# Performance work log

Measured on AMD Instinct MI355X. Metric: run time of the kernel, lower is better.

Reference implementation:

```python
import jax, jax.numpy as jnp
import numpy as np

N = 256
L = 1024
ALPHA = 0.5  # GBT_alpha: bilinear transform


def _hippo_legs(n):
    # HiPPO-LegS: A[i,k] = -sqrt(2i+1)sqrt(2k+1) if i>k; -(i+1) if i==k; 0 else
    q = np.arange(n, dtype=np.float64)
    r = np.sqrt(2.0 * q + 1.0)
    A = r[:, None] * r[None, :] * (q[:, None] > q[None, :])
    A = -(A + np.diag(q + 1.0))
    B = r[:, None]  # (N, 1)
    return A.astype(np.float32), B.astype(np.float32)


def setup_inputs() -> dict:
    key = jax.random.key(0)
    k_f, = jax.random.split(key, 1)
    A_np, B_np = _hippo_legs(N)
    return {
        "f": jax.random.normal(k_f, (L, 1), dtype=jnp.float32),
        "init_state": jnp.zeros((N, 1), dtype=jnp.float32),
        "A": jnp.asarray(A_np),
        "B": jnp.asarray(B_np),
    }


def reference(f, init_state, A, B):
    n = A.shape[0]
    seq_len = f.shape[0]
    C = jnp.ones((n,), dtype=jnp.float32)  # module's self.C
    I = jnp.eye(n, dtype=jnp.float32)

    # Per-step discretization: at step i (1-indexed), step_size = 1/i.
    step_sizes = 1.0 / jnp.arange(1, seq_len + 1, dtype=jnp.float32)  # (L,)

    def discretize(ss):
        # part1 = I - ss*alpha*A ; part2 = I + ss*(1-alpha)*A
        P1 = I - ss * ALPHA * A
        P2 = I + ss * (1.0 - ALPHA) * A
        # lstsq on an invertible square system == solve
        Ad = jnp.linalg.solve(P1, P2)          # (N, N)
        Bd = ss * jnp.linalg.solve(P1, B)      # (N, 1)
        return Ad, Bd

    GBT_A, GBT_B = jax.vmap(discretize)(step_sizes)  # (L,N,N), (L,N,1)

    f_scalar = f[:, 0]  # loop uses f[i-1][0]

    def step(c_prev, inp):
        Ad, Bd, fk = inp
        c = Ad @ c_prev + Bd * fk  # (N, 1)
        y = C @ c                  # (1,)
        return c, (c, y)

    _, (c_all, y_all) = jax.lax.scan(step, init_state, (GBT_A, GBT_B, f_scalar))
    # c_all: (L, N, 1) stacked hidden states; y_all: (L, 1)
    return c_all, y_all, GBT_A, GBT_B
```

## Files before the change

### kernel.cpp

```cpp
#include <hip/hip_runtime.h>

#define LSEQ 1024
#define NDIM 256

#define O_C 0
#define O_Y (LSEQ * NDIM)
#define O_A (O_Y + LSEQ)
#define O_B (O_A + (size_t)LSEQ * NDIM * NDIM)

#define RING 128
#define NGRP 136

typedef float v4f __attribute__((ext_vector_type(4)));

static __device__ __forceinline__ float frcp(float x) {
    return __builtin_amdgcn_rcpf(x);
}

static __device__ __forceinline__ float dpp_shr1(float inject, float src) {
    int r = __builtin_amdgcn_update_dpp(
        __float_as_int(inject), __float_as_int(src),
        0x138 , 0xF, 0xF, false);
    return __int_as_float(r);
}

__global__ __launch_bounds__(256) void hippo_main(
    const float* __restrict__ f,
    const float* __restrict__ init_state,
    const float* __restrict__ Bvec,
    float* __restrict__ out)
{
    const int tid = threadIdx.x;
    const int bid = blockIdx.x;

    if (bid == 0) {
        __shared__ float c_ring[RING * NDIM];
        __shared__ float y_lds[LSEQ];
        __shared__ float f_lds[LSEQ];

        for (int i = tid; i < LSEQ; i += 256) f_lds[i] = f[i];
        __syncthreads();

        if (tid < 64) {
            const int l = tid;
            float rr[4], cc[4];
            #pragma unroll
            for (int e = 0; e < 4; ++e) {
                rr[e] = Bvec[4 * l + e];
                cc[e] = init_state[4 * l + e];
            }
            const float base1 = (float)(4 * l + 1);

            float T = 0.0f, S = 0.0f, ssf = 0.0f, yacc = 0.0f;
            float fcur = f_lds[l];
            float fnxt = f_lds[64 + l];

            for (int grp = 0; grp <= NGRP; ++grp) {
                if (grp < NGRP) {
                    const int tb = grp * 8;
                    if ((tb & 63) == 0 && tb) {
                        fcur = fnxt;
                        int nb = tb + 64;
                        fnxt = f_lds[(nb < LSEQ ? nb : 0) + l];
                    }
                    const int fb = tb & 63;

                    #pragma unroll
                    for (int g = 0; g < 8; ++g) {
                        const int t = tb + g;
                        float ft = __int_as_float(
                            __builtin_amdgcn_readlane(__float_as_int(fcur), fb + g));

                        const int k0 = t - l;
                        const float h  = 0.5f * frcp((float)(k0 + 1));
                        const float h0 = 0.5f * frcp((float)(t + 1));
                        const float ssf0 = 2.0f * h0 * ft;

                        T    = dpp_shr1(0.0f, T);
                        S    = dpp_shr1(0.0f, S);
                        yacc = dpp_shr1(0.0f, yacc);
                        ssf  = dpp_shr1(ssf0, ssf);

                        if (k0 >= 0 && k0 < LSEQ) {
                            #pragma unroll
                            for (int e = 0; e < 4; ++e) {
                                float d    = fmaf(h, base1 + (float)e, 1.0f);
                                float invd = frcp(d);
                                float w = fmaf(2.0f - d, cc[e],
                                               rr[e] * fmaf(-h, T, ssf));
                                T = fmaf(rr[e], cc[e], T);
                                float num = fmaf(-h * rr[e], S, w);
                                float cn  = num * invd;
                                S = fmaf(rr[e], cn, S);
                                cc[e] = cn;
                            }
                            yacc += (cc[0] + cc[1]) + (cc[2] + cc[3]);
                            const int slot = t & (RING - 1);
                            v4f cv = { cc[0], cc[1], cc[2], cc[3] };
                            *reinterpret_cast<v4f*>(
                                &c_ring[slot * NDIM + 4 * l]) = cv;
                            if (l == 63) y_lds[k0] = yacc;
                        }
                    }
                }
                __syncthreads();
            }
        } else {
            const int wave = tid >> 6;
            const int lane = tid & 63;
            for (int grp = 0; grp <= NGRP; ++grp) {
                const int tb = grp * 8;
                #pragma unroll
                for (int ri = 0; ri < 8; ++ri) {
                    if (ri / 3 != wave - 1) continue;
                    int r = tb - 71 + ri;
                    if (r < 0 || r >= LSEQ) continue;
                    int slot = (r + lane) & (RING - 1);
                    v4f d = *reinterpret_cast<const v4f*>(
                        &c_ring[slot * NDIM + 4 * lane]);
                    *reinterpret_cast<v4f*>(
                        out + O_C + (size_t)r * NDIM + 4 * lane) = d;
                    if (lane == 0) out[O_Y + r] = y_lds[r];
                }
                __syncthreads();
            }
        }
    } else {
        const int k = bid - 1;
        const int lane = tid & 63;
        const int wave = tid >> 6;
        const float kp = (float)(k + 1);
        const float ss = 1.0f / kp;
        const float h  = 0.5f * ss;

        __shared__ float s_r[NDIM], s_invd[NDIM], s_rowco[NDIM], s_g[NDIM], s_diag[NDIM];
        {
            int i = tid;
            float r    = Bvec[i];
            float d    = fmaf(h, (float)(i + 1), 1.0f);
            float invd = 1.0f / d;
            s_r[i]     = r;
            s_invd[i]  = invd;
            s_rowco[i] = -2.0f * h * r * invd;
            s_g[i]     = (1.0f - h * (float)i) * invd;
            s_diag[i]  = fmaf(2.0f, invd, -1.0f);
        }
        __syncthreads();

        {
            float Pi = 1.0f;
            for (int j = 0; j < NDIM - 1; ++j) {
                float gj = s_g[j];
                Pi *= (j < tid) ? gj : 1.0f;
            }
            float* outB = out + O_B + (size_t)k * NDIM;
            outB[tid] = ss * s_r[tid] * s_invd[tid] * Pi;
        }

        float colc[4], Scol[4] = {0.f, 0.f, 0.f, 0.f};
        #pragma unroll
        for (int e = 0; e < 4; ++e) {
            int j = 4 * lane + e;
            colc[e] = s_r[j] * s_invd[j];
        }

        const int i0 = wave * 64;
        for (int i = 0; i < i0; ++i) {
            float g = s_g[i];
            #pragma unroll
            for (int e = 0; e < 4; ++e) {
                int j = 4 * lane + e;
                if (j < i)       Scol[e] *= g;
                else if (j == i) Scol[e] = colc[e];
            }
        }
        float* outA = out + O_A + (size_t)k * (NDIM * NDIM) + 4 * lane;
        for (int i = i0; i < i0 + 64; ++i) {
            float rowco = s_rowco[i];
            float g     = s_g[i];
            float dg    = s_diag[i];
            float v[4];
            #pragma unroll
            for (int e = 0; e < 4; ++e) {
                int j = 4 * lane + e;
                if (j < i) {
                    v[e] = rowco * Scol[e];
                    Scol[e] *= g;
                } else if (j == i) {
                    v[e] = dg;
                    Scol[e] = colc[e];
                } else {
                    v[e] = 0.0f;
                }
            }
            v4f vv = { v[0], v[1], v[2], v[3] };
            __builtin_nontemporal_store(
                vv, reinterpret_cast<v4f*>(outA + (size_t)i * NDIM));
        }
    }
}

extern "C" void kernel_launch(void* const* d_in, const int* in_sizes, int n_in,
                              void* d_out, int out_size, void* d_ws, size_t ws_size,
                              hipStream_t stream) {
    (void)in_sizes; (void)n_in; (void)d_ws; (void)ws_size; (void)out_size;
    const float* f    = (const float*)d_in[0];
    const float* init = (const float*)d_in[1];
    const float* Bv   = (const float*)d_in[3];
    float* outp       = (float*)d_out;
    hippo_main<<<1 + LSEQ, 256, 0, stream>>>(f, init, Bv, outp);
}
```

Baseline: 449.5 us.

## Compute GBT products via log-space prefix scan and restructure scan ticks

The discretization blocks replace the sequential column-product recurrence and the O(N) per-thread product loop with a log2 prefix scan (wave shuffles plus a cross-wave combine), tracking sign and zero counts separately. Each matrix entry then comes from a single exp2 of a log difference. The serial scan wave is split into three phases so most groups skip the activity check, uses zero-fill DPP shifts, tracks the step denominator incrementally, and doubles the group size to halve barriers. The writer waves now use nontemporal stores. The log/exp2 path trades exact products for hardware-approximate transcendentals, which risks precision loss when products are tiny.

```diff
diff --git a/kernel.cpp b/kernel.cpp
--- a/kernel.cpp
+++ b/kernel.cpp
@@ -9,18 +9,29 @@
 #define O_B (O_A + (size_t)LSEQ * NDIM * NDIM)
 
 #define RING 128
-#define NGRP 136
+#define GT   16
+#define NGRP 68
 
 typedef float v4f __attribute__((ext_vector_type(4)));
 
 static __device__ __forceinline__ float frcp(float x) {
     return __builtin_amdgcn_rcpf(x);
 }
-
-static __device__ __forceinline__ float dpp_shr1(float inject, float src) {
+static __device__ __forceinline__ float hlog2(float x) {
+    return __builtin_amdgcn_logf(x);
+}
+static __device__ __forceinline__ float hexp2(float x) {
+    return __builtin_amdgcn_exp2f(x);
+}
+
+static __device__ __forceinline__ float dpp_shr1_z(float x) {
     int r = __builtin_amdgcn_update_dpp(
-        __float_as_int(inject), __float_as_int(src),
-        0x138 , 0xF, 0xF, false);
+        __float_as_int(x), __float_as_int(x), 0x138 , 0xF, 0xF, true);
+    return __int_as_float(r);
+}
+static __device__ __forceinline__ float dpp_shr1_inj(float inject, float src) {
+    int r = __builtin_amdgcn_update_dpp(
+        __float_as_int(inject), __float_as_int(src), 0x138, 0xF, 0xF, false);
     return __int_as_float(r);
 }
 
@@ -43,84 +54,100 @@
 
         if (tid < 64) {
             const int l = tid;
-            float rr[4], cc[4];
+            float rr[4], cc[4], baseE[4];
             #pragma unroll
             for (int e = 0; e < 4; ++e) {
                 rr[e] = Bvec[4 * l + e];
                 cc[e] = init_state[4 * l + e];
-            }
-            const float base1 = (float)(4 * l + 1);
-
+                baseE[e] = (float)(4 * l + 1 + e);
+            }
             float T = 0.0f, S = 0.0f, ssf = 0.0f, yacc = 0.0f;
+            float E = (float)(-2 * l);
             float fcur = f_lds[l];
             float fnxt = f_lds[64 + l];
-
+            float ssfv = fcur * frcp((float)(l + 1));
+
+#define SCAN_TICK(T_, PHASE)                                                  \
+  {                                                                           \
+    const int t_ = (T_);                                                      \
+    float inj = __int_as_float(__builtin_amdgcn_readlane(                     \
+        __float_as_int(ssfv), t_ & 63));                                      \
+    T    = dpp_shr1_z(T);                                                     \
+    S    = dpp_shr1_z(S);                                                     \
+    yacc = dpp_shr1_z(yacc);                                                  \
+    ssf  = dpp_shr1_inj(inj, ssf);                                            \
+    E += 2.0f;                                                                \
+    float h = frcp(E);                                                        \
+    bool act = (PHASE == 1) ||                                                \
+               ((PHASE == 0) ? (t_ >= l) : (t_ - l < LSEQ));                  \
+    if (act) {                                                                \
+      _Pragma("unroll")                                                       \
+      for (int e = 0; e < 4; ++e) {                                           \
+        float d    = fmaf(h, baseE[e], 1.0f);                                 \
+        float invd = frcp(d);                                                 \
+        float w    = fmaf(2.0f - d, cc[e], rr[e] * fmaf(-h, T, ssf));         \
+        T = fmaf(rr[e], cc[e], T);                                            \
+        float num = fmaf(-h * rr[e], S, w);                                   \
+        float cn  = num * invd;                                               \
+        S = fmaf(rr[e], cn, S);                                               \
+        cc[e] = cn;                                                           \
+      }                                                                       \
+      yacc += (cc[0] + cc[1]) + (cc[2] + cc[3]);                              \
+      v4f cv = { cc[0], cc[1], cc[2], cc[3] };                                \
+      *reinterpret_cast<v4f*>(&c_ring[(t_ & (RING - 1)) * NDIM + 4 * l]) = cv;\
+      if (l == 63) y_lds[t_ - 63] = yacc;                                     \
+    }                                                                         \
+  }
+
+            int grp = 0;
+            for (; grp < 4; ++grp) {
+                const int tb = grp * GT;
+                #pragma unroll
+                for (int g = 0; g < GT; ++g) SCAN_TICK(tb + g, 0);
+                __syncthreads();
+            }
+            for (; grp < 64; ++grp) {
+                const int tb = grp * GT;
+                if ((tb & 63) == 0) {
+                    fcur = fnxt;
+                    int idx = tb + 64 + l;
+                    fnxt = f_lds[(idx < LSEQ) ? idx : 0];
+                    ssfv = fcur * frcp((float)(tb + l + 1));
+                }
+                #pragma unroll
+                for (int g = 0; g < GT; ++g) SCAN_TICK(tb + g, 1);
+                __syncthreads();
+            }
+            for (; grp < NGRP; ++grp) {
+                const int tb = grp * GT;
+                #pragma unroll
+                for (int g = 0; g < GT; ++g) SCAN_TICK(tb + g, 2);
+                __syncthreads();
+            }
+            __syncthreads();
+#undef SCAN_TICK
+        } else {
+            const int wv = tid >> 6;
+            const int lane = tid & 63;
             for (int grp = 0; grp <= NGRP; ++grp) {
-                if (grp < NGRP) {
-                    const int tb = grp * 8;
-                    if ((tb & 63) == 0 && tb) {
-                        fcur = fnxt;
-                        int nb = tb + 64;
-                        fnxt = f_lds[(nb < LSEQ ? nb : 0) + l];
-                    }
-                    const int fb = tb & 63;
-
-                    #pragma unroll
-                    for (int g = 0; g < 8; ++g) {
-                        const int t = tb + g;
-                        float ft = __int_as_float(
-                            __builtin_amdgcn_readlane(__float_as_int(fcur), fb + g));
-
-                        const int k0 = t - l;
-                        const float h  = 0.5f * frcp((float)(k0 + 1));
-                        const float h0 = 0.5f * frcp((float)(t + 1));
-                        const float ssf0 = 2.0f * h0 * ft;
-
-                        T    = dpp_shr1(0.0f, T);
-                        S    = dpp_shr1(0.0f, S);
-                        yacc = dpp_shr1(0.0f, yacc);
-                        ssf  = dpp_shr1(ssf0, ssf);
-
-                        if (k0 >= 0 && k0 < LSEQ) {
-                            #pragma unroll
-                            for (int e = 0; e < 4; ++e) {
-                                float d    = fmaf(h, base1 + (float)e, 1.0f);
-                                float invd = frcp(d);
-                                float w = fmaf(2.0f - d, cc[e],
-                                               rr[e] * fmaf(-h, T, ssf));
-                                T = fmaf(rr[e], cc[e], T);
-                                float num = fmaf(-h * rr[e], S, w);
-                                float cn  = num * invd;
-                                S = fmaf(rr[e], cn, S);
-                                cc[e] = cn;
-                            }
-                            yacc += (cc[0] + cc[1]) + (cc[2] + cc[3]);
-                            const int slot = t & (RING - 1);
-                            v4f cv = { cc[0], cc[1], cc[2], cc[3] };
-                            *reinterpret_cast<v4f*>(
-                                &c_ring[slot * NDIM + 4 * l]) = cv;
-                            if (l == 63) y_lds[k0] = yacc;
-                        }
+                const int r0 = grp * GT - 80;
+                const int lo = (wv == 1) ? 0 : (wv == 2) ? 6 : 11;
+                const int hi = (wv == 1) ? 5 : (wv == 2) ? 10 : 15;
+                for (int ri = lo; ri <= hi; ++ri) {
+                    int r = r0 + ri;
+                    if (r >= 0 && r < LSEQ) {
+                        int slot = (r + lane) & (RING - 1);
+                        v4f dv = *reinterpret_cast<const v4f*>(
+                            &c_ring[slot * NDIM + 4 * lane]);
+                        __builtin_nontemporal_store(dv,
+                            reinterpret_cast<v4f*>(
+                                out + O_C + (size_t)r * NDIM + 4 * lane));
                     }
                 }
-                __syncthreads();
-            }
-        } else {
-            const int wave = tid >> 6;
-            const int lane = tid & 63;
-            for (int grp = 0; grp <= NGRP; ++grp) {
-                const int tb = grp * 8;
-                #pragma unroll
-                for (int ri = 0; ri < 8; ++ri) {
-                    if (ri / 3 != wave - 1) continue;
-                    int r = tb - 71 + ri;
-                    if (r < 0 || r >= LSEQ) continue;
-                    int slot = (r + lane) & (RING - 1);
-                    v4f d = *reinterpret_cast<const v4f*>(
-                        &c_ring[slot * NDIM + 4 * lane]);
-                    *reinterpret_cast<v4f*>(
-                        out + O_C + (size_t)r * NDIM + 4 * lane) = d;
-                    if (lane == 0) out[O_Y + r] = y_lds[r];
+                if (wv == 3 && lane < GT) {
+                    int r = r0 + lane;
+                    if (r >= 0 && r < LSEQ)
+                        __builtin_nontemporal_store(y_lds[r], out + O_Y + r);
                 }
                 __syncthreads();
             }
@@ -133,69 +160,83 @@
         const float ss = 1.0f / kp;
         const float h  = 0.5f * ss;
 
-        __shared__ float s_r[NDIM], s_invd[NDIM], s_rowco[NDIM], s_g[NDIM], s_diag[NDIM];
+        __shared__ float s_cc[NDIM], s_rowco[NDIM], s_diag[NDIM], s_Lp[NDIM];
+        __shared__ int   s_NZp[NDIM];
+        __shared__ float s_wL[4];
+        __shared__ int   s_wNZ[4];
+
+        const int i = tid;
+        const float r    = Bvec[i];
+        const float dd   = fmaf(h, (float)(i + 1), 1.0f);
+        const float invd = 1.0f / dd;
+        const float g    = (1.0f - h * (float)i) * invd;
+
+        const int zer = (g == 0.0f) ? 1 : 0;
+        const int neg = (g < 0.0f) ? 1 : 0;
+        float sL = zer ? 0.0f : hlog2(fabsf(g));
+        int   sNZ = neg | (zer << 16);
+
+        #pragma unroll
+        for (int off = 1; off < 64; off <<= 1) {
+            float tL  = __shfl_up(sL, off);
+            int   tNZ = __shfl_up(sNZ, off);
+            if (lane >= off) { sL += tL; sNZ += tNZ; }
+        }
+        if (lane == 63) { s_wL[wave] = sL; s_wNZ[wave] = sNZ; }
+        __syncthreads();
+        for (int ww = 0; ww < wave; ++ww) { sL += s_wL[ww]; sNZ += s_wNZ[ww]; }
+
+        s_Lp[i]    = sL;
+        s_NZp[i]   = sNZ;
+        s_cc[i]    = r * invd;
+        s_rowco[i] = -2.0f * h * r * invd;
+        s_diag[i]  = fmaf(2.0f, invd, -1.0f);
+        __syncthreads();
+
         {
-            int i = tid;
-            float r    = Bvec[i];
-            float d    = fmaf(h, (float)(i + 1), 1.0f);
-            float invd = 1.0f / d;
-            s_r[i]     = r;
-            s_invd[i]  = invd;
-            s_rowco[i] = -2.0f * h * r * invd;
-            s_g[i]     = (1.0f - h * (float)i) * invd;
-            s_diag[i]  = fmaf(2.0f, invd, -1.0f);
-        }
-        __syncthreads();
-
-        {
-            float Pi = 1.0f;
-            for (int j = 0; j < NDIM - 1; ++j) {
-                float gj = s_g[j];
-                Pi *= (j < tid) ? gj : 1.0f;
-            }
-            float* outB = out + O_B + (size_t)k * NDIM;
-            outB[tid] = ss * s_r[tid] * s_invd[tid] * Pi;
-        }
-
-        float colc[4], Scol[4] = {0.f, 0.f, 0.f, 0.f};
+            float P;
+            if (i == 0) P = 1.0f;
+            else {
+                float Lw = s_Lp[i - 1]; int nzw = s_NZp[i - 1];
+                P = (nzw >> 16) ? 0.0f : hexp2(Lw);
+                if (nzw & 1) P = -P;
+            }
+            out[O_B + (size_t)k * NDIM + i] = -s_rowco[i] * P;
+        }
+
+        float Lj[4], ccj[4]; int NZj[4];
         #pragma unroll
         for (int e = 0; e < 4; ++e) {
             int j = 4 * lane + e;
-            colc[e] = s_r[j] * s_invd[j];
+            Lj[e]  = s_Lp[j];
+            NZj[e] = s_NZp[j];
+            ccj[e] = s_cc[j];
         }
 
         const int i0 = wave * 64;
-        for (int i = 0; i < i0; ++i) {
-            float g = s_g[i];
-            #pragma unroll
-            for (int e = 0; e < 4; ++e) {
-                int j = 4 * lane + e;
-                if (j < i)       Scol[e] *= g;
-                else if (j == i) Scol[e] = colc[e];
-            }
-        }
         float* outA = out + O_A + (size_t)k * (NDIM * NDIM) + 4 * lane;
-        for (int i = i0; i < i0 + 64; ++i) {
-            float rowco = s_rowco[i];
-            float g     = s_g[i];
-            float dg    = s_diag[i];
+        #pragma unroll 4
+        for (int ir = 0; ir < 64; ++ir) {
+            const int irow = i0 + ir;
+            const int ip = (irow > 0) ? (irow - 1) : 0;
+            const float Lpi = s_Lp[ip];
+            const int   NZi = s_NZp[ip];
+            const float rc  = s_rowco[irow];
+            const float dg  = s_diag[irow];
             float v[4];
             #pragma unroll
             for (int e = 0; e < 4; ++e) {
-                int j = 4 * lane + e;
-                if (j < i) {
-                    v[e] = rowco * Scol[e];
-                    Scol[e] *= g;
-                } else if (j == i) {
-                    v[e] = dg;
-                    Scol[e] = colc[e];
-                } else {
-                    v[e] = 0.0f;
-                }
+                const int j = 4 * lane + e;
+                float wv = hexp2(Lpi - Lj[e]);
+                int nzd = NZi - NZj[e];
+                wv = (nzd >> 16) ? 0.0f : wv;
+                wv = (nzd & 1) ? -wv : wv;
+                float val = rc * ccj[e] * wv;
+                v[e] = (j < irow) ? val : ((j == irow) ? dg : 0.0f);
             }
             v4f vv = { v[0], v[1], v[2], v[3] };
             __builtin_nontemporal_store(
-                vv, reinterpret_cast<v4f*>(outA + (size_t)i * NDIM));
+                vv, reinterpret_cast<v4f*>(outA + (size_t)irow * NDIM));
         }
     }
 }
```

Measured after the change: 383.6 us. 1.17x faster.
